# Kernel tuning notes

Measured on AMD Instinct MI355X. Metric: run time of the kernel, lower is better.

Reference implementation:

```python
import jax, jax.numpy as jnp
from jax import lax
import numpy as np

K = 4            # prototypes per class: 3 kmeans centroids + 1 backbone
EPS = 0.1        # sinkhorn entropic regularization
MAX_ITER = 100
THRESH = 0.01
KM_ITERS = 10    # Lloyd iterations (replaces host-side sklearn KMeans)
HW = 28          # the original reshapes pred to 28x28, fixing n = 784


def setup_inputs():
    key = jax.random.key(0)
    k1, k2, k3, k4 = jax.random.split(key, 4)
    b, n, d, c = 32, HW * HW, 1024, 20
    return {
        "query": jax.random.normal(k1, (b, n, d), dtype=jnp.float32),
        "score": jax.random.uniform(k2, (b, n, c), dtype=jnp.float32),
        "label": jax.random.randint(k3, (b, c), 0, 2),
        "gt": jax.random.randint(k4, (b, HW, HW), 0, c + 1),
        "weights": jnp.array([1.0, 1.0, 0.0, -1.0], dtype=jnp.float32),
    }


def _assign(dq, cen, selfm):
    # dq [b,m,d], cen [b,c,j,d], selfm [b,c,m] float mask -> one-hot labels, counts
    x2 = jnp.sum(dq * dq, axis=-1)                                   # [b,m]
    d2 = (x2[:, None, :, None]
          - 2.0 * jnp.einsum('bmd,bcjd->bcmj', dq, cen)
          + jnp.sum(cen * cen, axis=-1)[:, :, None, :])              # [b,c,m,j]
    oh = jax.nn.one_hot(jnp.argmin(d2, axis=-1), cen.shape[2], dtype=dq.dtype) * selfm[..., None]
    return oh, oh.sum(axis=2)


def _sinkhorn(Km, u, v):
    # vectorized over the [b,c] pair grid, per-pair early exit as in the torch loop
    def cond(st):
        it, r, cc, done = st
        return (it < MAX_ITER) & jnp.logical_not(jnp.all(done))

    def body(st):
        it, r, cc, done = st
        r1 = u / jnp.einsum('bcnj,bcj->bcn', Km, cc)
        c1 = v / jnp.einsum('bcnj,bcn->bcj', Km, r1)
        err = jnp.mean(jnp.abs(r1 - r), axis=-1)                     # [b,c]
        r = jnp.where(done[..., None], r, r1)
        cc = jnp.where(done[..., None], cc, c1)
        done = done | (err < THRESH)
        return it + 1, r, cc, done

    st = (jnp.int32(0), jnp.ones_like(u), jnp.ones_like(v),
          jnp.zeros(Km.shape[:2], dtype=bool))
    _, r, cc, _ = lax.while_loop(cond, body, st)
    return r[..., :, None] * cc[..., None, :] * Km                   # [b,c,n,K]


def _forward(query, score, label, gt, weights):
    b, n, d = query.shape
    c = score.shape[2]
    dq, ds = query[:, ::2, :], score[:, ::2, :]                      # stride-2 downsample
    m = dq.shape[1]
    cls_assign = jnp.argmax(ds, axis=-1)                             # [b,m]
    sel = cls_assign[:, None, :] == jnp.arange(c)[None, :, None]     # [b,c,m]
    selfm = sel.astype(query.dtype)
    cnt = selfm.sum(-1)                                              # [b,c]
    valid = (label > 0) & (cnt >= K)

    # ---- masked Lloyd's k-means with k-1 = 3 clusters per (image, class) pair
    order = jnp.argsort((~sel).astype(jnp.int32), axis=-1)           # masked points first
    init_idx = order[..., :K - 1]                                    # [b,c,3]
    cen = dq[jnp.arange(b)[:, None, None], init_idx]                 # [b,c,3,d]

    def km_step(cen, _):
        oh, kcnt = _assign(dq, cen, selfm)
        sums = jnp.einsum('bmd,bcmj->bcjd', dq, oh)
        cen = jnp.where(kcnt[..., None] > 0,
                        sums / jnp.maximum(kcnt, 1.0)[..., None], cen)
        return cen, None

    cen, _ = lax.scan(km_step, cen, None, length=KM_ITERS)
    oh, kcnt = _assign(dq, cen, selfm)                               # final labels

    # ---- sort centroids by mean cluster score (descending)
    sm = ds.mean(axis=-1)                                            # [b,m]
    avg = jnp.where(kcnt > 0,
                    jnp.einsum('bm,bcmj->bcj', sm, oh) / jnp.maximum(kcnt, 1.0),
                    -jnp.inf)
    ordj = jnp.argsort(-avg, axis=-1)                                # [b,c,3]
    cen = jnp.take_along_axis(cen, ordj[..., None], axis=2)

    # ---- backbone prototype = mean over unselected downsampled tokens
    un = 1.0 - selfm
    backbone = jnp.einsum('bmd,bcm->bcd', dq, un) / jnp.maximum(m - cnt, 1.0)[..., None]
    protos = jnp.concatenate([cen, backbone[:, :, None, :]], axis=2)  # [b,c,4,d]

    # ---- OT between query[0] tokens and the 4 prototypes (original uses query[0] always)
    q0 = query[0]
    q0h = q0 / jnp.maximum(jnp.linalg.norm(q0, axis=-1, keepdims=True), 1e-12)
    ph = protos / jnp.maximum(jnp.linalg.norm(protos, axis=-1, keepdims=True), 1e-12)
    sim = jnp.einsum('nd,bcjd->bcnj', q0h, ph)                       # [b,c,n,4]
    Km = lax.stop_gradient(jnp.exp(-(1.0 - sim) / EPS))              # torch.no_grad
    u = jnp.full((b, c, n), 1.0 / n, dtype=query.dtype)
    v = jnp.full((b, c, K), 1.0 / K, dtype=query.dtype)
    T = lax.stop_gradient(_sinkhorn(Km, u, v))                       # [b,c,n,4]

    valid = valid & jnp.logical_not(jnp.any(jnp.isnan(T), axis=(2, 3)))
    pred = jnp.einsum('bcnj,j->bcn', T, weights)                     # [b,c,n]

    # ---- BCE vs gt masks (28x28 -> 28x28 bilinear resize is the identity)
    y = (gt.reshape(b, -1)[:, None, :] == (jnp.arange(c) + 1)[None, :, None]).astype(pred.dtype)
    p = jnp.clip(pred, 0.0, 1.0)
    bce = -(y * jnp.maximum(jnp.log(p), -100.0)
            + (1.0 - y) * jnp.maximum(jnp.log(1.0 - p), -100.0)).mean(axis=-1)  # [b,c]
    bce = jnp.where(valid, bce, 0.0)
    total_n = valid.sum().astype(pred.dtype)
    return bce.sum() / (total_n + 1e-4)


def reference(query, score, label, gt, weights):
    return _forward(query, score, label, gt, weights)
```

## Files before the change

### kernel.cpp

```cpp
#include <hip/hip_runtime.h>
#include <cmath>

#define BB 32
#define NN 784
#define MM 392
#define DD 1024
#define CC 20
#define JJ 3
#define KP 4
#define KM_ITERS 10
#define GMAX 64

__global__ void k_cls(const float* __restrict__ score, int* __restrict__ cls,
                      float* __restrict__ sm, int* __restrict__ cnt) {
  int t = blockIdx.x * blockDim.x + threadIdx.x;
  if (t >= BB * MM) return;
  int b = t / MM, i = t - b * MM;
  const float* s = score + ((size_t)b * NN + 2 * i) * CC;
  float best = s[0]; int bi = 0; float acc = s[0];
  #pragma unroll
  for (int c = 1; c < CC; c++) { float v = s[c]; acc += v; if (v > best) { best = v; bi = c; } }
  cls[t] = bi;
  sm[t] = acc / (float)CC;
  atomicAdd(&cnt[b * CC + bi], 1);
}

__global__ void k_valid(const int* __restrict__ label, const int* __restrict__ cnt,
                        int* __restrict__ vlist, int* __restrict__ cpos, int* __restrict__ nvp) {
  __shared__ int sf[1024];
  int t = threadIdx.x;
  int flag = 0;
  if (t < BB * CC) flag = (label[t] > 0 && cnt[t] >= KP) ? 1 : 0;
  sf[t] = flag;
  __syncthreads();
  for (int off = 1; off < 1024; off <<= 1) {
    int v = sf[t];
    int add = (t >= off) ? sf[t - off] : 0;
    __syncthreads();
    sf[t] = v + add;
    __syncthreads();
  }
  if (t < BB * CC) {
    int pos = sf[t] - flag;
    cpos[t] = flag ? pos : -1;
    if (flag) vlist[pos] = t;
  }
  if (t == 0) *nvp = sf[BB * CC - 1];
}

__global__ __launch_bounds__(512) void k_gram(
    const float* __restrict__ query, const int* __restrict__ cls,
    const int* __restrict__ cpos, float* __restrict__ G,
    int* __restrict__ glist, int* __restrict__ gmcnt,
    float* __restrict__ classsum) {
  int bc = blockIdx.x; int b = bc / CC, c = bc - b * CC;
  int tid = threadIdx.x, lane = tid & 63, wv = tid >> 6;
  const float* qb = query + (size_t)b * NN * DD;
  __shared__ int s_scan[512];
  __shared__ int s_list[GMAX];
  __shared__ float s_acc[8][DD];
  int flag = 0;
  if (tid < MM) flag = (cls[b * MM + tid] == c) ? 1 : 0;
  s_scan[tid] = flag;
  __syncthreads();
  for (int off = 1; off < 512; off <<= 1) {
    int v = s_scan[tid];
    int add = (tid >= off) ? s_scan[tid - off] : 0;
    __syncthreads();
    s_scan[tid] = v + add;
    __syncthreads();
  }
  if (tid < MM && flag) { int p = s_scan[tid] - 1; if (p < GMAX) s_list[p] = tid; }
  __syncthreads();
  int mc = s_scan[MM - 1]; if (mc > GMAX) mc = GMAX;
  if (tid < mc) glist[bc * GMAX + tid] = s_list[tid];
  if (tid == 0) gmcnt[bc] = mc;
  int p = cpos[bc];
  bool valid = (p >= 0);
  float* Gb = G + (size_t)(valid ? p : 0) * (GMAX * GMAX);
  float4 acc[4];
  #pragma unroll
  for (int u = 0; u < 4; u++) acc[u] = make_float4(0.f, 0.f, 0.f, 0.f);
  for (int i = wv; i < mc; i += 8) {
    const float* ri = qb + (size_t)(2 * s_list[i]) * DD;
    float4 R[4];
    #pragma unroll
    for (int u = 0; u < 4; u++) R[u] = *(const float4*)(ri + lane * 4 + u * 256);
    #pragma unroll
    for (int u = 0; u < 4; u++) {
      acc[u].x += R[u].x; acc[u].y += R[u].y; acc[u].z += R[u].z; acc[u].w += R[u].w;
    }
    if (valid) {
      for (int ip = i; ip < mc; ip += 2) {
        int ip1 = ip + 1; bool has2 = ip1 < mc;
        const float* r0 = qb + (size_t)(2 * s_list[ip]) * DD;
        const float* r1 = qb + (size_t)(2 * s_list[has2 ? ip1 : ip]) * DD;
        float d0 = 0.f, d1 = 0.f;
        #pragma unroll
        for (int u = 0; u < 4; u++) {
          float4 v0 = *(const float4*)(r0 + lane * 4 + u * 256);
          float4 v1 = *(const float4*)(r1 + lane * 4 + u * 256);
          d0 += R[u].x * v0.x + R[u].y * v0.y + R[u].z * v0.z + R[u].w * v0.w;
          d1 += R[u].x * v1.x + R[u].y * v1.y + R[u].z * v1.z + R[u].w * v1.w;
        }
        for (int o = 1; o < 64; o <<= 1) {
          d0 += __shfl_xor(d0, o, 64);
          d1 += __shfl_xor(d1, o, 64);
        }
        if (lane == 0) {
          Gb[i * GMAX + ip] = d0; Gb[ip * GMAX + i] = d0;
          if (has2) { Gb[i * GMAX + ip1] = d1; Gb[ip1 * GMAX + i] = d1; }
        }
      }
    }
  }
  #pragma unroll
  for (int u = 0; u < 4; u++) *(float4*)&s_acc[wv][lane * 4 + u * 256] = acc[u];
  __syncthreads();
  float csx = 0.f, csy = 0.f;
  #pragma unroll
  for (int w = 0; w < 8; w++) {
    float2 t = *(const float2*)&s_acc[w][tid * 2];
    csx += t.x; csy += t.y;
  }
  float2 cso; cso.x = csx; cso.y = csy;
  *(float2*)(classsum + (size_t)bc * DD + tid * 2) = cso;
}

__global__ __launch_bounds__(64) void k_kmg(
    const float* __restrict__ G, const int* __restrict__ cpos,
    const int* __restrict__ gmcnt, const int* __restrict__ glist,
    const float* __restrict__ sm, float* __restrict__ wsort) {
  int bc = blockIdx.x;
  int p = cpos[bc];
  if (p < 0) return;
  int b = bc / CC;
  int lane = threadIdx.x;
  __shared__ float Gl[GMAX * 65];
  __shared__ float s_w[JJ][GMAX];
  int mc = gmcnt[bc];
  const float* Gg = G + (size_t)p * (GMAX * GMAX);
  for (int i = 0; i < mc; i++) Gl[i * 65 + lane] = Gg[i * GMAX + lane];
  bool act = lane < mc;
  int gidx = act ? glist[bc * GMAX + lane] : 0;
  float smv = act ? sm[b * MM + gidx] : 0.f;
  s_w[0][lane] = (lane == 0) ? 1.f : 0.f;
  s_w[1][lane] = (lane == 1) ? 1.f : 0.f;
  s_w[2][lane] = (lane == 2) ? 1.f : 0.f;
  __syncthreads();
  int aj = 0, n0 = 0, n1 = 0, n2 = 0;
  for (int it = 0; it <= KM_ITERS; it++) {
    float h0 = 0.f, h1 = 0.f, h2 = 0.f;
    if (act) {
      for (int i = 0; i < mc; i++) {
        float g = Gl[lane * 65 + i];
        h0 += s_w[0][i] * g; h1 += s_w[1][i] * g; h2 += s_w[2][i] * g;
      }
    }
    float t0 = s_w[0][lane] * h0, t1 = s_w[1][lane] * h1, t2 = s_w[2][lane] * h2;
    for (int o = 1; o < 64; o <<= 1) {
      t0 += __shfl_xor(t0, o, 64); t1 += __shfl_xor(t1, o, 64); t2 += __shfl_xor(t2, o, 64);
    }
    float e0 = t0 - 2.f * h0, e1 = t1 - 2.f * h1, e2 = t2 - 2.f * h2;
    aj = 0; float bv = e0;
    if (e1 < bv) { bv = e1; aj = 1; }
    if (e2 < bv) { bv = e2; aj = 2; }
    n0 = __popcll(__ballot(act && aj == 0));
    n1 = __popcll(__ballot(act && aj == 1));
    n2 = __popcll(__ballot(act && aj == 2));
    if (it == KM_ITERS) break;
    __syncthreads();
    if (act) {
      if (n0 > 0) s_w[0][lane] = (aj == 0) ? 1.f / (float)n0 : 0.f;
      if (n1 > 0) s_w[1][lane] = (aj == 1) ? 1.f / (float)n1 : 0.f;
      if (n2 > 0) s_w[2][lane] = (aj == 2) ? 1.f / (float)n2 : 0.f;
    }
    __syncthreads();
  }
  float s0 = (act && aj == 0) ? smv : 0.f;
  float s1 = (act && aj == 1) ? smv : 0.f;
  float s2 = (act && aj == 2) ? smv : 0.f;
  for (int o = 1; o < 64; o <<= 1) {
    s0 += __shfl_xor(s0, o, 64); s1 += __shfl_xor(s1, o, 64); s2 += __shfl_xor(s2, o, 64);
  }
  float avg[JJ];
  avg[0] = (n0 > 0) ? s0 / (float)n0 : -INFINITY;
  avg[1] = (n1 > 0) ? s1 / (float)n1 : -INFINITY;
  avg[2] = (n2 > 0) ? s2 / (float)n2 : -INFINITY;
  int ordv[JJ]; bool used[JJ] = {false, false, false};
  for (int s = 0; s < JJ; s++) {
    int bi = -1; float bv = 0.f;
    for (int j = 0; j < JJ; j++)
      if (!used[j] && (bi < 0 || avg[j] > bv)) { bi = j; bv = avg[j]; }
    used[bi] = true; ordv[s] = bi;
  }
  __syncthreads();
  float* wp = wsort + (size_t)p * (JJ * GMAX);
  wp[0 * GMAX + lane] = s_w[ordv[0]][lane];
  wp[1 * GMAX + lane] = s_w[ordv[1]][lane];
  wp[2 * GMAX + lane] = s_w[ordv[2]][lane];
}

__global__ __launch_bounds__(256) void k_cen(
    const float* __restrict__ query, const int* __restrict__ cpos,
    const int* __restrict__ gmcnt, const int* __restrict__ glist,
    const float* __restrict__ wsort, const float* __restrict__ totalsum,
    const float* __restrict__ classsum, const int* __restrict__ cnt,
    float* __restrict__ ph) {
  int bc = blockIdx.x; int p = cpos[bc];
  if (p < 0) return;
  int b = bc / CC;
  int tid = threadIdx.x, lane = tid & 63, wv = tid >> 6;
  __shared__ float s_wl[JJ][GMAX];
  __shared__ int s_gl[GMAX];
  __shared__ float s_red[4][4];
  __shared__ float s_nrm[4];
  int mc = gmcnt[bc];
  if (tid < JJ * GMAX) s_wl[tid >> 6][tid & 63] = wsort[(size_t)p * (JJ * GMAX) + tid];
  if (tid < GMAX) s_gl[tid] = (tid < mc) ? glist[bc * GMAX + tid] : 0;
  __syncthreads();
  const float* qb = query + (size_t)b * NN * DD;
  float4 a0 = make_float4(0.f, 0.f, 0.f, 0.f), a1 = a0, a2 = a0;
  for (int g = 0; g < mc; g++) {
    float4 v = *(const float4*)(qb + (size_t)(2 * s_gl[g]) * DD + tid * 4);
    float w0 = s_wl[0][g], w1 = s_wl[1][g], w2 = s_wl[2][g];
    a0.x += w0 * v.x; a0.y += w0 * v.y; a0.z += w0 * v.z; a0.w += w0 * v.w;
    a1.x += w1 * v.x; a1.y += w1 * v.y; a1.z += w1 * v.z; a1.w += w1 * v.w;
    a2.x += w2 * v.x; a2.y += w2 * v.y; a2.z += w2 * v.z; a2.w += w2 * v.w;
  }
  float denom = fmaxf((float)(MM - cnt[bc]), 1.f);
  float4 tv = *(const float4*)(totalsum + (size_t)b * DD + tid * 4);
  float4 cv = *(const float4*)(classsum + (size_t)bc * DD + tid * 4);
  float4 a3 = make_float4((tv.x - cv.x) / denom, (tv.y - cv.y) / denom,
                          (tv.z - cv.z) / denom, (tv.w - cv.w) / denom);
  float pp0 = a0.x * a0.x + a0.y * a0.y + a0.z * a0.z + a0.w * a0.w;
  float pp1 = a1.x * a1.x + a1.y * a1.y + a1.z * a1.z + a1.w * a1.w;
  float pp2 = a2.x * a2.x + a2.y * a2.y + a2.z * a2.z + a2.w * a2.w;
  float pp3 = a3.x * a3.x + a3.y * a3.y + a3.z * a3.z + a3.w * a3.w;
  for (int o = 1; o < 64; o <<= 1) {
    pp0 += __shfl_xor(pp0, o, 64); pp1 += __shfl_xor(pp1, o, 64);
    pp2 += __shfl_xor(pp2, o, 64); pp3 += __shfl_xor(pp3, o, 64);
  }
  if (lane == 0) { s_red[wv][0] = pp0; s_red[wv][1] = pp1; s_red[wv][2] = pp2; s_red[wv][3] = pp3; }
  __syncthreads();
  if (tid < 4)
    s_nrm[tid] = fmaxf(sqrtf(s_red[0][tid] + s_red[1][tid] + s_red[2][tid] + s_red[3][tid]), 1e-12f);
  __syncthreads();
  float n0 = s_nrm[0], n1 = s_nrm[1], n2 = s_nrm[2], n3 = s_nrm[3];
  *(float4*)(ph + ((size_t)bc * KP + 0) * DD + tid * 4) =
      make_float4(a0.x / n0, a0.y / n0, a0.z / n0, a0.w / n0);
  *(float4*)(ph + ((size_t)bc * KP + 1) * DD + tid * 4) =
      make_float4(a1.x / n1, a1.y / n1, a1.z / n1, a1.w / n1);
  *(float4*)(ph + ((size_t)bc * KP + 2) * DD + tid * 4) =
      make_float4(a2.x / n2, a2.y / n2, a2.z / n2, a2.w / n2);
  *(float4*)(ph + ((size_t)bc * KP + 3) * DD + tid * 4) =
      make_float4(a3.x / n3, a3.y / n3, a3.z / n3, a3.w / n3);
}

__global__ void k_totalsum(const float* __restrict__ classsum, float* __restrict__ totalsum) {
  int t = blockIdx.x * 256 + threadIdx.x;
  int b = t >> 10, k = t & (DD - 1);
  float s = 0.f;
  for (int c = 0; c < CC; c++) s += classsum[((size_t)b * CC + c) * DD + k];
  totalsum[t] = s;
}

__global__ void k_q0h(const float* __restrict__ query, float* __restrict__ q0h) {
  int n = blockIdx.x;
  const float* src = query + (size_t)n * DD;
  float ss = 0.f;
  for (int k = threadIdx.x; k < DD; k += 64) { float v = src[k]; ss += v * v; }
  for (int o = 32; o > 0; o >>= 1) ss += __shfl_xor(ss, o, 64);
  float nrm = fmaxf(sqrtf(ss), 1e-12f);
  for (int k = threadIdx.x; k < DD; k += 64) q0h[(size_t)n * DD + k] = src[k] / nrm;
}

__global__ __launch_bounds__(256) void k_gemm(const float* __restrict__ A,
    const float* __restrict__ ph, const int* __restrict__ vlist,
    const int* __restrict__ nvp, float* __restrict__ P) {
  int nv4 = 4 * *nvp;
  int n0 = blockIdx.y * 64;
  if (n0 >= nv4) return;
  __shared__ float As[64][20];
  __shared__ float Bs[64][20];
  int tx = threadIdx.x & 15, ty = threadIdx.x >> 4;
  int m0 = blockIdx.x * 64;
  int s = blockIdx.z;
  int lrow = threadIdx.x >> 2;
  int lk = (threadIdx.x & 3) * 4;
  int brow = n0 + lrow;
  bool bval = brow < nv4;
  const float* Brow = ph;
  if (bval) {
    int bcc = brow >> 2;
    Brow = ph + ((size_t)vlist[bcc] * KP + (brow & 3)) * DD;
  }
  float acc[4][4] = {};
  int kbase = s * 512;
  for (int k0 = kbase; k0 < kbase + 512; k0 += 16) {
    int ar = m0 + lrow;
    float4 av = (ar < NN) ? *(const float4*)(A + (size_t)ar * DD + k0 + lk)
                          : make_float4(0.f, 0.f, 0.f, 0.f);
    *(float4*)&As[lrow][lk] = av;
    float4 bv = bval ? *(const float4*)(Brow + k0 + lk)
                     : make_float4(0.f, 0.f, 0.f, 0.f);
    *(float4*)&Bs[lrow][lk] = bv;
    __syncthreads();
    #pragma unroll
    for (int kk = 0; kk < 16; kk += 4) {
      float4 a4[4], b4[4];
      #pragma unroll
      for (int i = 0; i < 4; i++) a4[i] = *(const float4*)&As[ty * 4 + i][kk];
      #pragma unroll
      for (int j = 0; j < 4; j++) b4[j] = *(const float4*)&Bs[tx + 16 * j][kk];
      #pragma unroll
      for (int i = 0; i < 4; i++)
        #pragma unroll
        for (int j = 0; j < 4; j++) {
          acc[i][j] += a4[i].x * b4[j].x;
          acc[i][j] += a4[i].y * b4[j].y;
          acc[i][j] += a4[i].z * b4[j].z;
          acc[i][j] += a4[i].w * b4[j].w;
        }
    }
    __syncthreads();
  }
  #pragma unroll
  for (int i = 0; i < 4; i++) {
    int mr = m0 + ty * 4 + i;
    if (mr >= NN) continue;
    float* row = P + ((size_t)s * NN + mr) * (size_t)(BB * CC * KP) + n0 + tx;
    #pragma unroll
    for (int j = 0; j < 4; j++) row[16 * j] = acc[i][j];
  }
}

__global__ void k_kred(const float* __restrict__ P, const int* __restrict__ nvp,
                       float* __restrict__ Km) {
  int nv = *nvp;
  int m = blockIdx.x;
  const float4* p0 = (const float4*)(P + (size_t)m * (BB * CC * KP));
  const float4* p1 = (const float4*)(P + ((size_t)NN + m) * (BB * CC * KP));
  for (int bcc = threadIdx.x; bcc < nv; bcc += 256) {
    float4 a = p0[bcc], bvv = p1[bcc];
    float4 o;
    o.x = expf(-(1.0f - (a.x + bvv.x)) / 0.1f);
    o.y = expf(-(1.0f - (a.y + bvv.y)) / 0.1f);
    o.z = expf(-(1.0f - (a.z + bvv.z)) / 0.1f);
    o.w = expf(-(1.0f - (a.w + bvv.w)) / 0.1f);
    *((float4*)Km + (size_t)bcc * NN + m) = o;
  }
}

__global__ __launch_bounds__(256) void k_sink(const float* __restrict__ Km,
    const int* __restrict__ label, const int* __restrict__ cnt,
    const int* __restrict__ cpos,
    const int* __restrict__ gt, const float* __restrict__ wts,
    float* __restrict__ bce, int* __restrict__ vld) {
  int bc = blockIdx.x; int b = bc / CC, c = bc - b * CC;
  if (label[bc] <= 0 || cnt[bc] < KP) {
    if (threadIdx.x == 0) { bce[bc] = 0.f; vld[bc] = 0; }
    return;
  }
  __shared__ __align__(16) float4 Ks[NN];
  __shared__ float r[NN];
  __shared__ float ccv[KP];
  __shared__ float wred[4][5];
  __shared__ float s_err;
  __shared__ int s_nan;
  const float4* Kg = (const float4*)Km + (size_t)cpos[bc] * NN;
  for (int t = threadIdx.x; t < NN; t += 256) { Ks[t] = Kg[t]; r[t] = 1.f; }
  if (threadIdx.x < KP) ccv[threadIdx.x] = 1.f;
  if (threadIdx.x == 0) s_nan = 0;
  __syncthreads();
  const float uu = 1.0f / (float)NN, vv = 1.0f / (float)KP;
  int lane = threadIdx.x & 63, wv = threadIdx.x >> 6;
  for (int it = 0; it < 100; it++) {
    float c0 = ccv[0], c1 = ccv[1], c2 = ccv[2], c3 = ccv[3];
    float dsum = 0.f, p0 = 0.f, p1 = 0.f, p2 = 0.f, p3 = 0.f;
    for (int n = threadIdx.x; n < NN; n += 256) {
      float4 kv = Ks[n];
      float S = kv.x * c0 + kv.y * c1 + kv.z * c2 + kv.w * c3;
      float r1 = uu / S;
      dsum += fabsf(r1 - r[n]);
      r[n] = r1;
      p0 += kv.x * r1; p1 += kv.y * r1; p2 += kv.z * r1; p3 += kv.w * r1;
    }
    for (int o = 32; o > 0; o >>= 1) {
      dsum += __shfl_down(dsum, o, 64);
      p0 += __shfl_down(p0, o, 64); p1 += __shfl_down(p1, o, 64);
      p2 += __shfl_down(p2, o, 64); p3 += __shfl_down(p3, o, 64);
    }
    if (lane == 0) { wred[wv][0] = dsum; wred[wv][1] = p0; wred[wv][2] = p1; wred[wv][3] = p2; wred[wv][4] = p3; }
    __syncthreads();
    if (threadIdx.x == 0) {
      float d = 0.f, q0 = 0.f, q1 = 0.f, q2 = 0.f, q3 = 0.f;
      for (int w = 0; w < 4; w++) { d += wred[w][0]; q0 += wred[w][1]; q1 += wred[w][2]; q2 += wred[w][3]; q3 += wred[w][4]; }
      ccv[0] = vv / q0; ccv[1] = vv / q1; ccv[2] = vv / q2; ccv[3] = vv / q3;
      s_err = d / (float)NN;
    }
    __syncthreads();
    if (s_err < 0.01f) break;
  }
  float w0 = wts[0], w1 = wts[1], w2 = wts[2], w3 = wts[3];
  float cc0 = ccv[0], cc1 = ccv[1], cc2 = ccv[2], cc3 = ccv[3];
  float bsum = 0.f; int nanloc = 0;
  const int* gtb = gt + b * NN;
  for (int n = threadIdx.x; n < NN; n += 256) {
    float4 kv = Ks[n];
    float rv = r[n];
    float T0 = rv * cc0 * kv.x, T1 = rv * cc1 * kv.y, T2 = rv * cc2 * kv.z, T3 = rv * cc3 * kv.w;
    if (T0 != T0 || T1 != T1 || T2 != T2 || T3 != T3) nanloc = 1;
    float pred = T0 * w0 + T1 * w1 + T2 * w2 + T3 * w3;
    float p = fminf(fmaxf(pred, 0.f), 1.f);
    float t = (gtb[n] == c + 1) ? fmaxf(logf(p), -100.f) : fmaxf(logf(1.f - p), -100.f);
    bsum += t;
  }
  if (nanloc) s_nan = 1;
  for (int o = 32; o > 0; o >>= 1) bsum += __shfl_down(bsum, o, 64);
  if (lane == 0) wred[wv][0] = bsum;
  __syncthreads();
  if (threadIdx.x == 0) {
    float tot = wred[0][0] + wred[1][0] + wred[2][0] + wred[3][0];
    if (s_nan) { bce[bc] = 0.f; vld[bc] = 0; }
    else { bce[bc] = -(tot / (float)NN); vld[bc] = 1; }
  }
}

__global__ void k_final(const float* __restrict__ bce, const int* __restrict__ vld,
                        float* __restrict__ out) {
  __shared__ float rs[256];
  __shared__ float rc[256];
  float s = 0.f, cv = 0.f;
  for (int t = threadIdx.x; t < BB * CC; t += 256) { s += bce[t]; cv += (float)vld[t]; }
  rs[threadIdx.x] = s; rc[threadIdx.x] = cv; __syncthreads();
  for (int o = 128; o > 0; o >>= 1) {
    if (threadIdx.x < o) { rs[threadIdx.x] += rs[threadIdx.x + o]; rc[threadIdx.x] += rc[threadIdx.x + o]; }
    __syncthreads();
  }
  if (threadIdx.x == 0) out[0] = rs[0] / (rc[0] + 0.0001f);
}

extern "C" void kernel_launch(void* const* d_in, const int* in_sizes, int n_in,
                              void* d_out, int out_size, void* d_ws, size_t ws_size,
                              hipStream_t stream) {
  (void)in_sizes; (void)n_in; (void)out_size; (void)ws_size;
  const float* query = (const float*)d_in[0];
  const float* score = (const float*)d_in[1];
  const int*   label = (const int*)d_in[2];
  const int*   gt    = (const int*)d_in[3];
  const float* wts   = (const float*)d_in[4];
  float* ws = (float*)d_ws;

  size_t off = 0;
  int* cls = (int*)(ws + off);       off += (size_t)BB * MM;
  int* cnt = (int*)(ws + off);       off += (size_t)BB * CC;
  float* sm = ws + off;              off += (size_t)BB * MM;
  int* vlist = (int*)(ws + off);     off += (size_t)BB * CC;
  int* cpos = (int*)(ws + off);      off += (size_t)BB * CC;
  int* nvp = (int*)(ws + off);       off += 16;
  int* glist = (int*)(ws + off);     off += (size_t)BB * CC * GMAX;
  int* gmcnt = (int*)(ws + off);     off += (size_t)BB * CC;
  float* wsort = ws + off;           off += (size_t)BB * CC * JJ * GMAX;
  float* classsum = ws + off;        off += (size_t)BB * CC * DD;
  float* totalsum = ws + off;        off += (size_t)BB * DD;
  float* ph = ws + off;              off += (size_t)BB * CC * KP * DD;
  float* q0h = ws + off;             off += (size_t)NN * DD;
  float* P = ws + off;               off += (size_t)2 * NN * BB * CC * KP;
  float* Km = ws + off;              off += (size_t)BB * CC * NN * KP;
  float* bce = ws + off;             off += (size_t)BB * CC;
  int* vld = (int*)(ws + off);       off += (size_t)BB * CC;
  float* G = P;

  hipMemsetAsync(cnt, 0, (size_t)BB * CC * sizeof(int), stream);
  k_cls<<<(BB * MM + 255) / 256, 256, 0, stream>>>(score, cls, sm, cnt);
  k_valid<<<1, 1024, 0, stream>>>(label, cnt, vlist, cpos, nvp);
  k_gram<<<BB * CC, 512, 0, stream>>>(query, cls, cpos, G, glist, gmcnt, classsum);
  k_kmg<<<BB * CC, 64, 0, stream>>>(G, cpos, gmcnt, glist, sm, wsort);
  k_totalsum<<<(BB * DD) / 256, 256, 0, stream>>>(classsum, totalsum);
  k_cen<<<BB * CC, 256, 0, stream>>>(query, cpos, gmcnt, glist, wsort, totalsum,
                                     classsum, cnt, ph);
  k_q0h<<<NN, 64, 0, stream>>>(query, q0h);
  dim3 gg((NN + 63) / 64, (BB * CC * KP) / 64, 2);
  k_gemm<<<gg, 256, 0, stream>>>(q0h, ph, vlist, nvp, P);
  k_kred<<<NN, 256, 0, stream>>>(P, nvp, Km);
  k_sink<<<BB * CC, 256, 0, stream>>>(Km, label, cnt, cpos, gt, wts, bce, vld);
  k_final<<<1, 256, 0, stream>>>(bce, vld, (float*)d_out);
}
```

Before: 314.0 us.

## Fuse Gram build with k-means and fold exp reduction into Sinkhorn kernel

```diff
diff --git a/kernel.cpp b/kernel.cpp
--- a/kernel.cpp
+++ b/kernel.cpp
@@ -10,6 +10,7 @@
 #define KP 4
 #define KM_ITERS 10
 #define GMAX 64
+#define SKK 3
 
 __global__ void k_cls(const float* __restrict__ score, int* __restrict__ cls,
                       float* __restrict__ sm, int* __restrict__ cnt) {
@@ -50,15 +51,18 @@
 
 __global__ __launch_bounds__(512) void k_gram(
     const float* __restrict__ query, const int* __restrict__ cls,
-    const int* __restrict__ cpos, float* __restrict__ G,
+    const int* __restrict__ cpos, const float* __restrict__ sm,
     int* __restrict__ glist, int* __restrict__ gmcnt,
-    float* __restrict__ classsum) {
+    float* __restrict__ classsum, float* __restrict__ wsort) {
   int bc = blockIdx.x; int b = bc / CC, c = bc - b * CC;
   int tid = threadIdx.x, lane = tid & 63, wv = tid >> 6;
   const float* qb = query + (size_t)b * NN * DD;
   __shared__ int s_scan[512];
   __shared__ int s_list[GMAX];
-  __shared__ float s_acc[8][DD];
+  __shared__ __align__(16) float Xs[GMAX][68];
+  __shared__ float Gl[GMAX][65];
+  __shared__ float s_w[JJ][GMAX];
+
   int flag = 0;
   if (tid < MM) flag = (cls[b * MM + tid] == c) ? 1 : 0;
   s_scan[tid] = flag;
@@ -70,90 +74,76 @@
     s_scan[tid] = v + add;
     __syncthreads();
   }
-  if (tid < MM && flag) { int p = s_scan[tid] - 1; if (p < GMAX) s_list[p] = tid; }
+  if (tid < MM && flag) { int pp = s_scan[tid] - 1; if (pp < GMAX) s_list[pp] = tid; }
   __syncthreads();
   int mc = s_scan[MM - 1]; if (mc > GMAX) mc = GMAX;
   if (tid < mc) glist[bc * GMAX + tid] = s_list[tid];
   if (tid == 0) gmcnt[bc] = mc;
-  int p = cpos[bc];
-  bool valid = (p >= 0);
-  float* Gb = G + (size_t)(valid ? p : 0) * (GMAX * GMAX);
-  float4 acc[4];
+  bool valid = (cpos[bc] >= 0);
+
+  int npairs = mc * (mc + 1) / 2;
+  int pi[5], pj[5];
+  float pacc[5];
   #pragma unroll
-  for (int u = 0; u < 4; u++) acc[u] = make_float4(0.f, 0.f, 0.f, 0.f);
-  for (int i = wv; i < mc; i += 8) {
-    const float* ri = qb + (size_t)(2 * s_list[i]) * DD;
-    float4 R[4];
+  for (int s = 0; s < 5; s++) {
+    pacc[s] = 0.f; pi[s] = -1; pj[s] = 0;
+    int p = tid + s * 512;
+    if (valid && p < npairs) {
+      int i = (int)floorf((sqrtf(8.0f * (float)p + 1.0f) - 1.0f) * 0.5f);
+      while ((i + 1) * (i + 2) / 2 <= p) i++;
+      while (i * (i + 1) / 2 > p) i--;
+      pi[s] = i; pj[s] = p - i * (i + 1) / 2;
+    }
+  }
+
+  for (int ch = 0; ch < DD / 64; ch++) {
+    __syncthreads();
+    for (int e = tid; e < mc * 16; e += 512) {
+      int row = e >> 4, c4 = e & 15;
+      float4 v = *(const float4*)(qb + (size_t)(2 * s_list[row]) * DD + ch * 64 + c4 * 4);
+      *(float4*)&Xs[row][c4 * 4] = v;
+    }
+    __syncthreads();
     #pragma unroll
-    for (int u = 0; u < 4; u++) R[u] = *(const float4*)(ri + lane * 4 + u * 256);
-    #pragma unroll
-    for (int u = 0; u < 4; u++) {
-      acc[u].x += R[u].x; acc[u].y += R[u].y; acc[u].z += R[u].z; acc[u].w += R[u].w;
-    }
-    if (valid) {
-      for (int ip = i; ip < mc; ip += 2) {
-        int ip1 = ip + 1; bool has2 = ip1 < mc;
-        const float* r0 = qb + (size_t)(2 * s_list[ip]) * DD;
-        const float* r1 = qb + (size_t)(2 * s_list[has2 ? ip1 : ip]) * DD;
-        float d0 = 0.f, d1 = 0.f;
+    for (int s = 0; s < 5; s++) {
+      if (pi[s] >= 0) {
+        const float4* xi = (const float4*)&Xs[pi[s]][0];
+        const float4* xj = (const float4*)&Xs[pj[s]][0];
+        float a = 0.f;
         #pragma unroll
-        for (int u = 0; u < 4; u++) {
-          float4 v0 = *(const float4*)(r0 + lane * 4 + u * 256);
-          float4 v1 = *(const float4*)(r1 + lane * 4 + u * 256);
-          d0 += R[u].x * v0.x + R[u].y * v0.y + R[u].z * v0.z + R[u].w * v0.w;
-          d1 += R[u].x * v1.x + R[u].y * v1.y + R[u].z * v1.z + R[u].w * v1.w;
+        for (int kk = 0; kk < 16; kk++) {
+          float4 u = xi[kk], w = xj[kk];
+          a += u.x * w.x + u.y * w.y + u.z * w.z + u.w * w.w;
         }
-        for (int o = 1; o < 64; o <<= 1) {
-          d0 += __shfl_xor(d0, o, 64);
-          d1 += __shfl_xor(d1, o, 64);
-        }
-        if (lane == 0) {
-          Gb[i * GMAX + ip] = d0; Gb[ip * GMAX + i] = d0;
-          if (has2) { Gb[i * GMAX + ip1] = d1; Gb[ip1 * GMAX + i] = d1; }
-        }
+        pacc[s] += a;
       }
     }
-  }
+    if (tid < 64) {
+      float s = 0.f;
+      for (int row = 0; row < mc; row++) s += Xs[row][tid];
+      classsum[(size_t)bc * DD + ch * 64 + tid] = s;
+    }
+  }
+  if (!valid) return;
   #pragma unroll
-  for (int u = 0; u < 4; u++) *(float4*)&s_acc[wv][lane * 4 + u * 256] = acc[u];
-  __syncthreads();
-  float csx = 0.f, csy = 0.f;
-  #pragma unroll
-  for (int w = 0; w < 8; w++) {
-    float2 t = *(const float2*)&s_acc[w][tid * 2];
-    csx += t.x; csy += t.y;
-  }
-  float2 cso; cso.x = csx; cso.y = csy;
-  *(float2*)(classsum + (size_t)bc * DD + tid * 2) = cso;
-}
-
-__global__ __launch_bounds__(64) void k_kmg(
-    const float* __restrict__ G, const int* __restrict__ cpos,
-    const int* __restrict__ gmcnt, const int* __restrict__ glist,
-    const float* __restrict__ sm, float* __restrict__ wsort) {
-  int bc = blockIdx.x;
-  int p = cpos[bc];
-  if (p < 0) return;
-  int b = bc / CC;
-  int lane = threadIdx.x;
-  __shared__ float Gl[GMAX * 65];
-  __shared__ float s_w[JJ][GMAX];
-  int mc = gmcnt[bc];
-  const float* Gg = G + (size_t)p * (GMAX * GMAX);
-  for (int i = 0; i < mc; i++) Gl[i * 65 + lane] = Gg[i * GMAX + lane];
+  for (int s = 0; s < 5; s++)
+    if (pi[s] >= 0) { Gl[pi[s]][pj[s]] = pacc[s]; Gl[pj[s]][pi[s]] = pacc[s]; }
+  __syncthreads();
+
   bool act = lane < mc;
-  int gidx = act ? glist[bc * GMAX + lane] : 0;
-  float smv = act ? sm[b * MM + gidx] : 0.f;
-  s_w[0][lane] = (lane == 0) ? 1.f : 0.f;
-  s_w[1][lane] = (lane == 1) ? 1.f : 0.f;
-  s_w[2][lane] = (lane == 2) ? 1.f : 0.f;
+  float smv = act ? sm[b * MM + s_list[lane]] : 0.f;
+  if (wv == 0) {
+    s_w[0][lane] = (lane == 0) ? 1.f : 0.f;
+    s_w[1][lane] = (lane == 1) ? 1.f : 0.f;
+    s_w[2][lane] = (lane == 2) ? 1.f : 0.f;
+  }
   __syncthreads();
   int aj = 0, n0 = 0, n1 = 0, n2 = 0;
   for (int it = 0; it <= KM_ITERS; it++) {
     float h0 = 0.f, h1 = 0.f, h2 = 0.f;
     if (act) {
       for (int i = 0; i < mc; i++) {
-        float g = Gl[lane * 65 + i];
+        float g = Gl[lane][i];
         h0 += s_w[0][i] * g; h1 += s_w[1][i] * g; h2 += s_w[2][i] * g;
       }
     }
@@ -183,22 +173,31 @@
   for (int o = 1; o < 64; o <<= 1) {
     s0 += __shfl_xor(s0, o, 64); s1 += __shfl_xor(s1, o, 64); s2 += __shfl_xor(s2, o, 64);
   }
-  float avg[JJ];
-  avg[0] = (n0 > 0) ? s0 / (float)n0 : -INFINITY;
-  avg[1] = (n1 > 0) ? s1 / (float)n1 : -INFINITY;
-  avg[2] = (n2 > 0) ? s2 / (float)n2 : -INFINITY;
-  int ordv[JJ]; bool used[JJ] = {false, false, false};
-  for (int s = 0; s < JJ; s++) {
-    int bi = -1; float bv = 0.f;
-    for (int j = 0; j < JJ; j++)
-      if (!used[j] && (bi < 0 || avg[j] > bv)) { bi = j; bv = avg[j]; }
-    used[bi] = true; ordv[s] = bi;
-  }
-  __syncthreads();
-  float* wp = wsort + (size_t)p * (JJ * GMAX);
-  wp[0 * GMAX + lane] = s_w[ordv[0]][lane];
-  wp[1 * GMAX + lane] = s_w[ordv[1]][lane];
-  wp[2 * GMAX + lane] = s_w[ordv[2]][lane];
+  if (wv == 0) {
+    float avg[JJ];
+    avg[0] = (n0 > 0) ? s0 / (float)n0 : -INFINITY;
+    avg[1] = (n1 > 0) ? s1 / (float)n1 : -INFINITY;
+    avg[2] = (n2 > 0) ? s2 / (float)n2 : -INFINITY;
+    int ordv[JJ]; bool used[JJ] = {false, false, false};
+    for (int s = 0; s < JJ; s++) {
+      int bi = -1; float bv = 0.f;
+      for (int j = 0; j < JJ; j++)
+        if (!used[j] && (bi < 0 || avg[j] > bv)) { bi = j; bv = avg[j]; }
+      used[bi] = true; ordv[s] = bi;
+    }
+    float* wp = wsort + (size_t)cpos[bc] * (JJ * GMAX);
+    wp[0 * GMAX + lane] = s_w[ordv[0]][lane];
+    wp[1 * GMAX + lane] = s_w[ordv[1]][lane];
+    wp[2 * GMAX + lane] = s_w[ordv[2]][lane];
+  }
+}
+
+__global__ void k_totalsum(const float* __restrict__ classsum, float* __restrict__ totalsum) {
+  int t = blockIdx.x * 256 + threadIdx.x;
+  int b = t >> 10, k = t & (DD - 1);
+  float s = 0.f;
+  for (int c = 0; c < CC; c++) s += classsum[((size_t)b * CC + c) * DD + k];
+  totalsum[t] = s;
 }
 
 __global__ __launch_bounds__(256) void k_cen(
@@ -255,14 +254,6 @@
       make_float4(a2.x / n2, a2.y / n2, a2.z / n2, a2.w / n2);
   *(float4*)(ph + ((size_t)bc * KP + 3) * DD + tid * 4) =
       make_float4(a3.x / n3, a3.y / n3, a3.z / n3, a3.w / n3);
-}
-
-__global__ void k_totalsum(const float* __restrict__ classsum, float* __restrict__ totalsum) {
-  int t = blockIdx.x * 256 + threadIdx.x;
-  int b = t >> 10, k = t & (DD - 1);
-  float s = 0.f;
-  for (int c = 0; c < CC; c++) s += classsum[((size_t)b * CC + c) * DD + k];
-  totalsum[t] = s;
 }
 
 __global__ void k_q0h(const float* __restrict__ query, float* __restrict__ q0h) {
@@ -296,8 +287,9 @@
     Brow = ph + ((size_t)vlist[bcc] * KP + (brow & 3)) * DD;
   }
   float acc[4][4] = {};
-  int kbase = s * 512;
-  for (int k0 = kbase; k0 < kbase + 512; k0 += 16) {
+  int kbase = s * 352;
+  int kend = (kbase + 352 < DD) ? (kbase + 352) : DD;
+  for (int k0 = kbase; k0 < kend; k0 += 16) {
     int ar = m0 + lrow;
     float4 av = (ar < NN) ? *(const float4*)(A + (size_t)ar * DD + k0 + lk)
                           : make_float4(0.f, 0.f, 0.f, 0.f);
@@ -335,24 +327,7 @@
   }
 }
 
-__global__ void k_kred(const float* __restrict__ P, const int* __restrict__ nvp,
-                       float* __restrict__ Km) {
-  int nv = *nvp;
-  int m = blockIdx.x;
-  const float4* p0 = (const float4*)(P + (size_t)m * (BB * CC * KP));
-  const float4* p1 = (const float4*)(P + ((size_t)NN + m) * (BB * CC * KP));
-  for (int bcc = threadIdx.x; bcc < nv; bcc += 256) {
-    float4 a = p0[bcc], bvv = p1[bcc];
-    float4 o;
-    o.x = expf(-(1.0f - (a.x + bvv.x)) / 0.1f);
-    o.y = expf(-(1.0f - (a.y + bvv.y)) / 0.1f);
-    o.z = expf(-(1.0f - (a.z + bvv.z)) / 0.1f);
-    o.w = expf(-(1.0f - (a.w + bvv.w)) / 0.1f);
-    *((float4*)Km + (size_t)bcc * NN + m) = o;
-  }
-}
-
-__global__ __launch_bounds__(256) void k_sink(const float* __restrict__ Km,
+__global__ __launch_bounds__(256) void k_sink(const float* __restrict__ P,
     const int* __restrict__ label, const int* __restrict__ cnt,
     const int* __restrict__ cpos,
     const int* __restrict__ gt, const float* __restrict__ wts,
@@ -368,8 +343,19 @@
   __shared__ float wred[4][5];
   __shared__ float s_err;
   __shared__ int s_nan;
-  const float4* Kg = (const float4*)Km + (size_t)cpos[bc] * NN;
-  for (int t = threadIdx.x; t < NN; t += 256) { Ks[t] = Kg[t]; r[t] = 1.f; }
+  int p = cpos[bc];
+  const float4* P4 = (const float4*)P;
+  for (int t = threadIdx.x; t < NN; t += 256) {
+    float4 a = P4[(size_t)(0 * NN + t) * (BB * CC) + p];
+    float4 bb = P4[(size_t)(1 * NN + t) * (BB * CC) + p];
+    float4 cc3 = P4[(size_t)(2 * NN + t) * (BB * CC) + p];
+    float4 o;
+    o.x = expf(-(1.0f - (a.x + bb.x + cc3.x)) / 0.1f);
+    o.y = expf(-(1.0f - (a.y + bb.y + cc3.y)) / 0.1f);
+    o.z = expf(-(1.0f - (a.z + bb.z + cc3.z)) / 0.1f);
+    o.w = expf(-(1.0f - (a.w + bb.w + cc3.w)) / 0.1f);
+    Ks[t] = o; r[t] = 1.f;
+  }
   if (threadIdx.x < KP) ccv[threadIdx.x] = 1.f;
   if (threadIdx.x == 0) s_nan = 0;
   __syncthreads();
@@ -412,8 +398,8 @@
     float T0 = rv * cc0 * kv.x, T1 = rv * cc1 * kv.y, T2 = rv * cc2 * kv.z, T3 = rv * cc3 * kv.w;
     if (T0 != T0 || T1 != T1 || T2 != T2 || T3 != T3) nanloc = 1;
     float pred = T0 * w0 + T1 * w1 + T2 * w2 + T3 * w3;
-    float p = fminf(fmaxf(pred, 0.f), 1.f);
-    float t = (gtb[n] == c + 1) ? fmaxf(logf(p), -100.f) : fmaxf(logf(1.f - p), -100.f);
+    float pcl = fminf(fmaxf(pred, 0.f), 1.f);
+    float t = (gtb[n] == c + 1) ? fmaxf(logf(pcl), -100.f) : fmaxf(logf(1.f - pcl), -100.f);
     bsum += t;
   }
   if (nanloc) s_nan = 1;
@@ -466,24 +452,20 @@
   float* totalsum = ws + off;        off += (size_t)BB * DD;
   float* ph = ws + off;              off += (size_t)BB * CC * KP * DD;
   float* q0h = ws + off;             off += (size_t)NN * DD;
-  float* P = ws + off;               off += (size_t)2 * NN * BB * CC * KP;
-  float* Km = ws + off;              off += (size_t)BB * CC * NN * KP;
+  float* P = ws + off;               off += (size_t)SKK * NN * BB * CC * KP;
   float* bce = ws + off;             off += (size_t)BB * CC;
   int* vld = (int*)(ws + off);       off += (size_t)BB * CC;
-  float* G = P;
 
   hipMemsetAsync(cnt, 0, (size_t)BB * CC * sizeof(int), stream);
   k_cls<<<(BB * MM + 255) / 256, 256, 0, stream>>>(score, cls, sm, cnt);
   k_valid<<<1, 1024, 0, stream>>>(label, cnt, vlist, cpos, nvp);
-  k_gram<<<BB * CC, 512, 0, stream>>>(query, cls, cpos, G, glist, gmcnt, classsum);
-  k_kmg<<<BB * CC, 64, 0, stream>>>(G, cpos, gmcnt, glist, sm, wsort);
+  k_gram<<<BB * CC, 512, 0, stream>>>(query, cls, cpos, sm, glist, gmcnt, classsum, wsort);
   k_totalsum<<<(BB * DD) / 256, 256, 0, stream>>>(classsum, totalsum);
   k_cen<<<BB * CC, 256, 0, stream>>>(query, cpos, gmcnt, glist, wsort, totalsum,
                                      classsum, cnt, ph);
   k_q0h<<<NN, 64, 0, stream>>>(query, q0h);
-  dim3 gg((NN + 63) / 64, (BB * CC * KP) / 64, 2);
+  dim3 gg((NN + 63) / 64, (BB * CC * KP) / 64, SKK);
   k_gemm<<<gg, 256, 0, stream>>>(q0h, ph, vlist, nvp, P);
-  k_kred<<<NN, 256, 0, stream>>>(P, nvp, Km);
-  k_sink<<<BB * CC, 256, 0, stream>>>(Km, label, cnt, cpos, gt, wts, bce, vld);
+  k_sink<<<BB * CC, 256, 0, stream>>>(P, label, cnt, cpos, gt, wts, bce, vld);
   k_final<<<1, 256, 0, stream>>>(bce, vld, (float*)d_out);
 }
```

Result: faster. 296.3 us (-5.6%).
